# Kernel tuning notes

Measured on AMD Instinct MI355X. Metric: run time of the kernel, lower is better.

Reference implementation:

```python
import jax, jax.numpy as jnp
import numpy as np

B, N, H, W = 4, 4096, 480, 640
RADIUS = 2.0        # hard-coded self.radius in DiskLoss
SCORES_TH = 0.1     # PeakyLoss scores_th
KP_PENALTY = -0.001 # configs['kp_penalty']


def setup_inputs() -> dict:
    key = jax.random.key(0)
    ks = jax.random.split(key, 6)
    lp0 = jax.random.uniform(ks[0], (B, 1, H, W), dtype=jnp.float32)
    lp1 = jax.random.uniform(ks[1], (B, 1, H, W), dtype=jnp.float32)
    # keypoints are normalized grid_sample coords in [-1, 1], (x, y) order
    kp0 = jax.random.uniform(ks[2], (B, N, 2), dtype=jnp.float32) * 2.0 - 1.0
    kp1 = jax.random.uniform(ks[3], (B, N, 2), dtype=jnp.float32) * 2.0 - 1.0
    d0 = jax.random.uniform(ks[4], (B, N), dtype=jnp.float32)
    d1 = jax.random.uniform(ks[5], (B, N), dtype=jnp.float32)
    return dict(local_point0=lp0, local_point1=lp1, keypoints0=kp0,
                keypoints1=kp1, score_dispersity0=d0, score_dispersity1=d1)


def grid_sample_bilinear(img, pts):
    """torch.grid_sample(mode='bilinear', align_corners=True) for one image.
    img: [H, W]; pts: [N, 2] in [-1, 1], pts[:,0]=x (width), pts[:,1]=y (height)."""
    Hh, Ww = img.shape
    x = (pts[:, 0] + 1.0) * 0.5 * (Ww - 1)
    y = (pts[:, 1] + 1.0) * 0.5 * (Hh - 1)
    x0 = jnp.floor(x); y0 = jnp.floor(y)
    wx = x - x0; wy = y - y0
    def g(yy, xx):
        yi = jnp.clip(yy, 0, Hh - 1).astype(jnp.int32)
        xi = jnp.clip(xx, 0, Ww - 1).astype(jnp.int32)
        return img[yi, xi]
    return (g(y0, x0) * (1 - wx) * (1 - wy)
            + g(y0, x0 + 1) * wx * (1 - wy)
            + g(y0 + 1, x0) * (1 - wx) * wy
            + g(y0 + 1, x0 + 1) * wx * wy)


def nms_valid(kpts_wh, scores):
    """Faithful sequential NMS from compute_correspondence for one image.
    kpts_wh: [N, 2] pixel coords; scores: [N]. Returns bool [N] valid mask."""
    n = scores.shape[0]
    sq = jnp.sum(kpts_wh * kpts_wh, axis=-1)
    d2 = sq[:, None] + sq[None, :] - 2.0 * (kpts_wh @ kpts_wh.T)  # [N, N]
    local_mask = d2 < RADIUS * RADIUS
    valid_cnt0 = local_mask.sum(-1).astype(jnp.int32)
    need = valid_cnt0 > 1  # indices_need_nms (computed once, as in torch)
    idx = jnp.arange(n)
    neg_inf = jnp.asarray(-jnp.inf, scores.dtype)
    def body(i, vc):
        row = local_mask[i]
        cond = need[i] & (vc[i] > 0)
        j = jnp.argmax(jnp.where(row, scores, neg_inf))  # best-scoring neighbor
        suppressed = jnp.where(row & (idx != j), 0, vc)
        return jnp.where(cond, suppressed, vc)
    vc = jax.lax.fori_loop(0, n, body, valid_cnt0)
    return vc > 0


def stream_loss(local_point, kpts, disp):
    # local_point [B,1,H,W], kpts [B,N,2] in [-1,1], disp [B,N]
    wh = jnp.array([local_point.shape[3] - 1, local_point.shape[2] - 1],
                   dtype=local_point.dtype)
    scores = jax.vmap(lambda m, k: grid_sample_bilinear(m[0], k))(local_point, kpts)  # [B,N]
    kpts_wh = (kpts / 2.0 + 0.5) * wh  # pixel coords
    valid = jax.vmap(nms_valid)(jax.lax.stop_gradient(kpts_wh),
                                jax.lax.stop_gradient(scores))  # [B,N] bool
    # PeakyLoss over NMS-surviving keypoints with score > threshold
    peaky_mask = (valid & (scores > SCORES_TH)).astype(disp.dtype)
    cnt = jnp.maximum(peaky_mask.sum(), 1.0)
    loss_peaky = jnp.sum(disp * peaky_mask) / cnt
    # keypoint score term (kp_penalty-weighted mean of surviving scores)
    vmask = valid.astype(scores.dtype)
    vcnt = jnp.maximum(vmask.sum(), 1.0)
    score_mean = jnp.sum(scores * vmask) / vcnt
    return loss_peaky + KP_PENALTY * score_mean


def reference(local_point0, local_point1, keypoints0, keypoints1,
              score_dispersity0, score_dispersity1):
    return (stream_loss(local_point0, keypoints0, score_dispersity0)
            + stream_loss(local_point1, keypoints1, score_dispersity1))
```

## Files before the change

kernel.cpp:

```cpp
#include <hip/hip_runtime.h>
#include <math.h>

#define NN 4096
#define HH 480
#define WW 640
#define RAD2 4.0f
#define TH_SCORE 0.1f
#define KPPEN -0.001f
#define CXN 160
#define CYN 120
#define NCELL (CXN * CYN)
#define SLOTS 8
#define CAP 48

#define OFF_SCORES  0
#define OFF_PTS     131072
#define OFF_CNT     655360
#define OFF_PARTNER 688128
#define OFF_ROWS    753664
#define OFF_CELLS   1277952
#define OFF_CCNT    3735552
#define OFF_ACC     4349952
#define OFF_DONE    4349984

__global__ __launch_bounds__(256) void k_sample(
    const float* __restrict__ lp0, const float* __restrict__ lp1,
    const float* __restrict__ kp0, const float* __restrict__ kp1,
    float* __restrict__ scores, float4* __restrict__ pts,
    unsigned short* __restrict__ cells, unsigned int* __restrict__ ccnt)
{
#pragma clang fp contract(off)
    int gid = blockIdx.x * 256 + threadIdx.x;
    int s = gid >> 14;
    int r = gid & 16383;
    int b = r >> 12;
    const float* kp  = (s ? kp1 : kp0) + (size_t)r * 2;
    const float* img = (s ? lp1 : lp0) + (size_t)b * (HH * WW);
    float px = kp[0], py = kp[1];
    float x = (px + 1.0f) * 0.5f * (float)(WW - 1);
    float y = (py + 1.0f) * 0.5f * (float)(HH - 1);
    float x0 = floorf(x), y0 = floorf(y);
    float wx = x - x0, wy = y - y0;
    int ix0 = (int)fminf(fmaxf(x0, 0.0f), (float)(WW - 1));
    int iy0 = (int)fminf(fmaxf(y0, 0.0f), (float)(HH - 1));
    int ix1 = (int)fminf(fmaxf(x0 + 1.0f, 0.0f), (float)(WW - 1));
    int iy1 = (int)fminf(fmaxf(y0 + 1.0f, 0.0f), (float)(HH - 1));
    float g00 = img[iy0 * WW + ix0];
    float g01 = img[iy0 * WW + ix1];
    float g10 = img[iy1 * WW + ix0];
    float g11 = img[iy1 * WW + ix1];
    float sc = g00 * (1.0f - wx) * (1.0f - wy)
             + g01 * wx * (1.0f - wy)
             + g10 * (1.0f - wx) * wy
             + g11 * wx * wy;
    float xw = (px / 2.0f + 0.5f) * (float)(WW - 1);
    float yw = (py / 2.0f + 0.5f) * (float)(HH - 1);
    float sq = xw * xw + yw * yw;
    scores[gid] = sc;
    pts[gid] = make_float4(xw, yw, sq, 0.0f);
    int imgid = gid >> 12;
    int li = gid & (NN - 1);
    int cx = (int)(xw * 0.25f); cx = cx < 0 ? 0 : (cx > CXN - 1 ? CXN - 1 : cx);
    int cy = (int)(yw * 0.25f); cy = cy < 0 ? 0 : (cy > CYN - 1 ? CYN - 1 : cy);
    int cell = imgid * NCELL + cy * CXN + cx;
    unsigned int pos = atomicAdd(&ccnt[cell], 1u);
    if (pos < SLOTS) cells[(size_t)cell * SLOTS + pos] = (unsigned short)li;
}

__global__ __launch_bounds__(256) void k_cnt(
    const float4* __restrict__ pts, const unsigned short* __restrict__ cells,
    const unsigned int* __restrict__ ccnt,
    unsigned char* __restrict__ cnt, unsigned short* __restrict__ partner,
    uint4* __restrict__ rows4)
{
#pragma clang fp contract(off)
    int gid = blockIdx.x * 256 + threadIdx.x;
    int imgid = gid >> 12;
    int li = gid & (NN - 1);
    const float4* p = pts + ((size_t)imgid << 12);
    float4 a = p[li];
    int cx = (int)(a.x * 0.25f); cx = cx < 0 ? 0 : (cx > CXN - 1 ? CXN - 1 : cx);
    int cy = (int)(a.y * 0.25f); cy = cy < 0 ? 0 : (cy > CYN - 1 ? CYN - 1 : cy);

    int c = 0, sum = 0; bool ov = false;
    unsigned long long rlo = 0ull, rhi = 0ull;
    auto place = [&](int pos, unsigned q) {
        unsigned long long v = (unsigned long long)q;
        switch (pos) {
            case 0: rlo |= v;       break;
            case 1: rlo |= v << 16; break;
            case 2: rlo |= v << 32; break;
            case 3: rlo |= v << 48; break;
            case 4: rhi |= v;       break;
            case 5: rhi |= v << 16; break;
            case 6: rhi |= v << 32; break;
            case 7: rhi |= v << 48; break;
        }
    };
    auto test = [&](unsigned q) {
        float4 qq = p[q];
        float dot = a.x * qq.x + a.y * qq.y;
        float t = a.z + qq.z;
        float d2 = fmaf(-2.0f, dot, t);
        if (d2 < RAD2) {
            if (c < 8) place(c, q);
            ++c; sum += (int)q;
        }
    };

#pragma unroll
    for (int dy = -1; dy <= 1; ++dy) {
#pragma unroll
        for (int dx = -1; dx <= 1; ++dx) {
            int yy = cy + dy, xx = cx + dx;
            bool valid = (yy >= 0) & (yy < CYN) & (xx >= 0) & (xx < CXN);
            int cell = imgid * NCELL + (valid ? yy * CXN + xx : 0);
            unsigned n = valid ? ccnt[cell] : 0u;
            if (n > SLOTS) { ov = true; n = SLOTS; }
            uint4 cl = valid ? *(const uint4*)&cells[(size_t)cell * SLOTS]
                             : make_uint4(0, 0, 0, 0);
            unsigned q0 = cl.x & 0xffffu, q1 = cl.x >> 16;
            unsigned q2 = cl.y & 0xffffu, q3 = cl.y >> 16;
            unsigned q4 = cl.z & 0xffffu, q5 = cl.z >> 16;
            unsigned q6 = cl.w & 0xffffu, q7 = cl.w >> 16;
            if (n > 0) test(q0);
            if (n > 1) test(q1);
            if (n > 2) test(q2);
            if (n > 3) test(q3);
            if (n > 4) test(q4);
            if (n > 5) test(q5);
            if (n > 6) test(q6);
            if (n > 7) test(q7);
        }
    }
    if (ov) {
        c = 0; sum = 0; rlo = 0ull; rhi = 0ull;
        for (int j = 0; j < NN; ++j) test((unsigned)j);
    }
    cnt[gid] = (unsigned char)(c > 255 ? 255 : c);
    partner[gid] = (unsigned short)((sum - li) & 0xFFFF);
    if (c >= 3 && c <= 8)
        rows4[gid] = make_uint4((unsigned)rlo, (unsigned)(rlo >> 32),
                                (unsigned)rhi, (unsigned)(rhi >> 32));
}

__global__ __launch_bounds__(256) void k_nms(
    const float* __restrict__ scoresG, const float4* __restrict__ pts,
    const unsigned char* __restrict__ cntG, const unsigned short* __restrict__ partnerG,
    const uint4* __restrict__ rows4,
    const float* __restrict__ dd0, const float* __restrict__ dd1,
    float* __restrict__ acc, unsigned int* __restrict__ done,
    float* __restrict__ out)
{
#pragma clang fp contract(off)
    __shared__ float          s_sc[NN];
    __shared__ unsigned char  s_cnt[NN];
    __shared__ unsigned short s_partner[NN];
    __shared__ unsigned short s_mem[256][CAP + 2];
    __shared__ float s_red[4];

    int imgid = blockIdx.x >> 4;
    int seg = blockIdx.x & 15;
    int base = imgid << 12;
    int tid = threadIdx.x;
    const float4* p = pts + (size_t)base;

    for (int t = tid; t < NN; t += 256) {
        s_sc[t] = scoresG[base + t];
        s_cnt[t] = cntG[base + t];
        s_partner[t] = partnerG[base + t];
    }
    __syncthreads();

    int li = (seg << 8) + tid;
    int c = s_cnt[li];
    bool alive = true;

    if (c >= 2) {
        int pr = s_partner[li];
        if (c == 2 && s_cnt[pr] == 2) {
            int lo = li < pr ? li : pr, hi = li < pr ? pr : li;
            int w = (s_sc[lo] >= s_sc[hi]) ? lo : hi;
            alive = (w == li);
        } else {
            unsigned short* mem = s_mem[tid];
            int cntm = 1, proc = 0;
            mem[0] = (unsigned short)li;
            auto insert = [&](unsigned q) {
                for (int k = 0; k < cntm; ++k) if (mem[k] == (unsigned short)q) return;
                if (cntm < CAP) mem[cntm++] = (unsigned short)q;
            };
            auto full_insert = [&](int m) {
                float4 pm = p[m];
                for (int j = 0; j < NN; ++j) {
                    float4 qq = p[j];
                    float dot = pm.x * qq.x + pm.y * qq.y;
                    float t = pm.z + qq.z;
                    float d2 = fmaf(-2.0f, dot, t);
                    if (d2 < RAD2) insert((unsigned)j);
                }
            };
            while (proc < cntm) {
                int m = mem[proc++];
                int cm = s_cnt[m];
                if (cm == 2) {
                    insert(s_partner[m]);
                } else if (cm <= 8) {
                    uint4 w = rows4[base + m];
                    unsigned q0 = w.x & 0xffffu, q1 = w.x >> 16;
                    unsigned q2 = w.y & 0xffffu, q3 = w.y >> 16;
                    unsigned q4 = w.z & 0xffffu, q5 = w.z >> 16;
                    unsigned q6 = w.w & 0xffffu, q7 = w.w >> 16;
                    if (cm > 0) insert(q0);
                    if (cm > 1) insert(q1);
                    if (cm > 2) insert(q2);
                    if (cm > 3) insert(q3);
                    if (cm > 4) insert(q4);
                    if (cm > 5) insert(q5);
                    if (cm > 6) insert(q6);
                    if (cm > 7) insert(q7);
                } else {
                    full_insert(m);
                }
            }
            for (int k = 1; k < cntm; ++k) {
                unsigned short v = mem[k]; int j2 = k;
                while (j2 > 0 && mem[j2 - 1] > v) { mem[j2] = mem[j2 - 1]; --j2; }
                mem[j2] = v;
            }
            unsigned long long am = (cntm >= 64) ? ~0ull : ((1ull << cntm) - 1ull);
            auto clearbit = [&](unsigned q) {
                for (int k = 0; k < cntm; ++k)
                    if (mem[k] == (unsigned short)q) { am &= ~(1ull << k); return; }
            };
            for (int k = 0; k < cntm; ++k) {
                if (!((am >> k) & 1ull)) continue;
                int m = mem[k];
                int cm = s_cnt[m];
                if (cm == 2) {
                    int pr2 = s_partner[m];
                    int lo = m < pr2 ? m : pr2, hi = m < pr2 ? pr2 : m;
                    int w = (s_sc[lo] >= s_sc[hi]) ? lo : hi;
                    clearbit((unsigned)(w == lo ? hi : lo));
                } else if (cm <= 8) {
                    uint4 w = rows4[base + m];
                    unsigned q0 = w.x & 0xffffu, q1 = w.x >> 16;
                    unsigned q2 = w.y & 0xffffu, q3 = w.y >> 16;
                    unsigned q4 = w.z & 0xffffu, q5 = w.z >> 16;
                    unsigned q6 = w.w & 0xffffu, q7 = w.w >> 16;
                    float bs = -1.0f; int bi = NN;
                    auto cand = [&](int k2, unsigned q) {
                        if (k2 < cm) {
                            float s2 = s_sc[q];
                            if (s2 > bs || (s2 == bs && (int)q < bi)) { bs = s2; bi = (int)q; }
                        }
                    };
                    cand(0, q0); cand(1, q1); cand(2, q2); cand(3, q3);
                    cand(4, q4); cand(5, q5); cand(6, q6); cand(7, q7);
                    auto clr = [&](int k2, unsigned q) {
                        if (k2 < cm && (int)q != bi) clearbit(q);
                    };
                    clr(0, q0); clr(1, q1); clr(2, q2); clr(3, q3);
                    clr(4, q4); clr(5, q5); clr(6, q6); clr(7, q7);
                } else {
                    float4 pm = p[m];
                    float bs = -1.0f; int bi = NN;
                    for (int j = 0; j < NN; ++j) {
                        float4 qq = p[j];
                        float dot = pm.x * qq.x + pm.y * qq.y;
                        float t = pm.z + qq.z;
                        float d2 = fmaf(-2.0f, dot, t);
                        if (d2 < RAD2) {
                            float s2 = s_sc[j];
                            if (s2 > bs || (s2 == bs && j < bi)) { bs = s2; bi = j; }
                        }
                    }
                    for (int j = 0; j < NN; ++j) {
                        float4 qq = p[j];
                        float dot = pm.x * qq.x + pm.y * qq.y;
                        float t = pm.z + qq.z;
                        float d2 = fmaf(-2.0f, dot, t);
                        if (d2 < RAD2 && j != bi) clearbit((unsigned)j);
                    }
                }
            }
            for (int k = 0; k < cntm; ++k)
                if (mem[k] == (unsigned short)li) { alive = ((am >> k) & 1ull) != 0; break; }
        }
    }

    int stream = imgid >> 2, b = imgid & 3;
    const float* disp = (stream ? dd1 : dd0) + (size_t)b * NN;
    float sum_dp = 0.f, cnt_p = 0.f, sum_sv = 0.f, cnt_v = 0.f;
    if (alive) {
        float sc = s_sc[li];
        cnt_v = 1.0f; sum_sv = sc;
        if (sc > TH_SCORE) { cnt_p = 1.0f; sum_dp = disp[li]; }
    }
    __syncthreads();
#pragma unroll
    for (int q = 0; q < 4; ++q) {
        float v = (q == 0) ? sum_dp : (q == 1) ? cnt_p : (q == 2) ? sum_sv : cnt_v;
        for (int o = 32; o > 0; o >>= 1) v += __shfl_down(v, o, 64);
        if ((tid & 63) == 0) s_red[tid >> 6] = v;
        __syncthreads();
        if (tid == 0) {
            float r = s_red[0] + s_red[1] + s_red[2] + s_red[3];
            atomicAdd(&acc[stream * 4 + q], r);
        }
        __syncthreads();
    }

    if (tid == 0) {
        __threadfence();
        unsigned prev = atomicAdd(done, 1u);
        if (prev == 127u) {
            float r = 0.0f;
            for (int s = 0; s < 2; ++s) {
                float sdp = atomicAdd(&acc[s * 4 + 0], 0.0f);
                float cp  = atomicAdd(&acc[s * 4 + 1], 0.0f);
                float ssv = atomicAdd(&acc[s * 4 + 2], 0.0f);
                float cv  = atomicAdd(&acc[s * 4 + 3], 0.0f);
                r += sdp / fmaxf(cp, 1.0f) + KPPEN * (ssv / fmaxf(cv, 1.0f));
            }
            out[0] = r;
        }
    }
}

extern "C" void kernel_launch(void* const* d_in, const int* in_sizes, int n_in,
                              void* d_out, int out_size, void* d_ws, size_t ws_size,
                              hipStream_t stream)
{
    const float* lp0 = (const float*)d_in[0];
    const float* lp1 = (const float*)d_in[1];
    const float* kp0 = (const float*)d_in[2];
    const float* kp1 = (const float*)d_in[3];
    const float* dd0 = (const float*)d_in[4];
    const float* dd1 = (const float*)d_in[5];

    char* ws = (char*)d_ws;
    float*          scores  = (float*)(ws + OFF_SCORES);
    float4*         pts     = (float4*)(ws + OFF_PTS);
    unsigned char*  cnt     = (unsigned char*)(ws + OFF_CNT);
    unsigned short* partner = (unsigned short*)(ws + OFF_PARTNER);
    uint4*          rows4   = (uint4*)(ws + OFF_ROWS);
    unsigned short* cells   = (unsigned short*)(ws + OFF_CELLS);
    unsigned int*   ccnt    = (unsigned int*)(ws + OFF_CCNT);
    float*          acc     = (float*)(ws + OFF_ACC);
    unsigned int*   done    = (unsigned int*)(ws + OFF_DONE);

    hipMemsetAsync(ws + OFF_CCNT, 0, 614436, stream);
    k_sample<<<128, 256, 0, stream>>>(lp0, lp1, kp0, kp1, scores, pts, cells, ccnt);
    k_cnt<<<128, 256, 0, stream>>>(pts, cells, ccnt, cnt, partner, rows4);
    k_nms<<<128, 256, 0, stream>>>(scores, pts, cnt, partner, rows4,
                                   dd0, dd1, acc, done, (float*)d_out);
}
```

Baseline: 116.3 us.

## Fuse three NMS pipeline kernels into one cooperative kernel with grid syncs

Merges the sampling, neighbour-counting and NMS kernels into a single cooperative launch, using grid-wide syncs in place of kernel boundaries. The final reduction now runs after a last grid sync instead of through a done-counter atomic. The aim is to remove the launch gaps between three short kernels. In exchange it pays the cost of cooperative launch and grid barriers, and the large shared-memory footprint now applies to every phase.

```diff
diff --git a/kernel.cpp b/kernel.cpp
--- a/kernel.cpp
+++ b/kernel.cpp
@@ -1,5 +1,8 @@
 #include <hip/hip_runtime.h>
+#include <hip/hip_cooperative_groups.h>
 #include <math.h>
+
+namespace cg = cooperative_groups;
 
 #define NN 4096
 #define HH 480
@@ -12,6 +15,7 @@
 #define NCELL (CXN * CYN)
 #define SLOTS 8
 #define CAP 48
+#define NBLK 128
 
 #define OFF_SCORES  0
 #define OFF_PTS     131072
@@ -21,135 +25,15 @@
 #define OFF_CELLS   1277952
 #define OFF_CCNT    3735552
 #define OFF_ACC     4349952
-#define OFF_DONE    4349984
-
-__global__ __launch_bounds__(256) void k_sample(
+
+__global__ __launch_bounds__(256) void k_fused(
     const float* __restrict__ lp0, const float* __restrict__ lp1,
     const float* __restrict__ kp0, const float* __restrict__ kp1,
+    const float* __restrict__ dd0, const float* __restrict__ dd1,
     float* __restrict__ scores, float4* __restrict__ pts,
-    unsigned short* __restrict__ cells, unsigned int* __restrict__ ccnt)
-{
-#pragma clang fp contract(off)
-    int gid = blockIdx.x * 256 + threadIdx.x;
-    int s = gid >> 14;
-    int r = gid & 16383;
-    int b = r >> 12;
-    const float* kp  = (s ? kp1 : kp0) + (size_t)r * 2;
-    const float* img = (s ? lp1 : lp0) + (size_t)b * (HH * WW);
-    float px = kp[0], py = kp[1];
-    float x = (px + 1.0f) * 0.5f * (float)(WW - 1);
-    float y = (py + 1.0f) * 0.5f * (float)(HH - 1);
-    float x0 = floorf(x), y0 = floorf(y);
-    float wx = x - x0, wy = y - y0;
-    int ix0 = (int)fminf(fmaxf(x0, 0.0f), (float)(WW - 1));
-    int iy0 = (int)fminf(fmaxf(y0, 0.0f), (float)(HH - 1));
-    int ix1 = (int)fminf(fmaxf(x0 + 1.0f, 0.0f), (float)(WW - 1));
-    int iy1 = (int)fminf(fmaxf(y0 + 1.0f, 0.0f), (float)(HH - 1));
-    float g00 = img[iy0 * WW + ix0];
-    float g01 = img[iy0 * WW + ix1];
-    float g10 = img[iy1 * WW + ix0];
-    float g11 = img[iy1 * WW + ix1];
-    float sc = g00 * (1.0f - wx) * (1.0f - wy)
-             + g01 * wx * (1.0f - wy)
-             + g10 * (1.0f - wx) * wy
-             + g11 * wx * wy;
-    float xw = (px / 2.0f + 0.5f) * (float)(WW - 1);
-    float yw = (py / 2.0f + 0.5f) * (float)(HH - 1);
-    float sq = xw * xw + yw * yw;
-    scores[gid] = sc;
-    pts[gid] = make_float4(xw, yw, sq, 0.0f);
-    int imgid = gid >> 12;
-    int li = gid & (NN - 1);
-    int cx = (int)(xw * 0.25f); cx = cx < 0 ? 0 : (cx > CXN - 1 ? CXN - 1 : cx);
-    int cy = (int)(yw * 0.25f); cy = cy < 0 ? 0 : (cy > CYN - 1 ? CYN - 1 : cy);
-    int cell = imgid * NCELL + cy * CXN + cx;
-    unsigned int pos = atomicAdd(&ccnt[cell], 1u);
-    if (pos < SLOTS) cells[(size_t)cell * SLOTS + pos] = (unsigned short)li;
-}
-
-__global__ __launch_bounds__(256) void k_cnt(
-    const float4* __restrict__ pts, const unsigned short* __restrict__ cells,
-    const unsigned int* __restrict__ ccnt,
     unsigned char* __restrict__ cnt, unsigned short* __restrict__ partner,
-    uint4* __restrict__ rows4)
-{
-#pragma clang fp contract(off)
-    int gid = blockIdx.x * 256 + threadIdx.x;
-    int imgid = gid >> 12;
-    int li = gid & (NN - 1);
-    const float4* p = pts + ((size_t)imgid << 12);
-    float4 a = p[li];
-    int cx = (int)(a.x * 0.25f); cx = cx < 0 ? 0 : (cx > CXN - 1 ? CXN - 1 : cx);
-    int cy = (int)(a.y * 0.25f); cy = cy < 0 ? 0 : (cy > CYN - 1 ? CYN - 1 : cy);
-
-    int c = 0, sum = 0; bool ov = false;
-    unsigned long long rlo = 0ull, rhi = 0ull;
-    auto place = [&](int pos, unsigned q) {
-        unsigned long long v = (unsigned long long)q;
-        switch (pos) {
-            case 0: rlo |= v;       break;
-            case 1: rlo |= v << 16; break;
-            case 2: rlo |= v << 32; break;
-            case 3: rlo |= v << 48; break;
-            case 4: rhi |= v;       break;
-            case 5: rhi |= v << 16; break;
-            case 6: rhi |= v << 32; break;
-            case 7: rhi |= v << 48; break;
-        }
-    };
-    auto test = [&](unsigned q) {
-        float4 qq = p[q];
-        float dot = a.x * qq.x + a.y * qq.y;
-        float t = a.z + qq.z;
-        float d2 = fmaf(-2.0f, dot, t);
-        if (d2 < RAD2) {
-            if (c < 8) place(c, q);
-            ++c; sum += (int)q;
-        }
-    };
-
-#pragma unroll
-    for (int dy = -1; dy <= 1; ++dy) {
-#pragma unroll
-        for (int dx = -1; dx <= 1; ++dx) {
-            int yy = cy + dy, xx = cx + dx;
-            bool valid = (yy >= 0) & (yy < CYN) & (xx >= 0) & (xx < CXN);
-            int cell = imgid * NCELL + (valid ? yy * CXN + xx : 0);
-            unsigned n = valid ? ccnt[cell] : 0u;
-            if (n > SLOTS) { ov = true; n = SLOTS; }
-            uint4 cl = valid ? *(const uint4*)&cells[(size_t)cell * SLOTS]
-                             : make_uint4(0, 0, 0, 0);
-            unsigned q0 = cl.x & 0xffffu, q1 = cl.x >> 16;
-            unsigned q2 = cl.y & 0xffffu, q3 = cl.y >> 16;
-            unsigned q4 = cl.z & 0xffffu, q5 = cl.z >> 16;
-            unsigned q6 = cl.w & 0xffffu, q7 = cl.w >> 16;
-            if (n > 0) test(q0);
-            if (n > 1) test(q1);
-            if (n > 2) test(q2);
-            if (n > 3) test(q3);
-            if (n > 4) test(q4);
-            if (n > 5) test(q5);
-            if (n > 6) test(q6);
-            if (n > 7) test(q7);
-        }
-    }
-    if (ov) {
-        c = 0; sum = 0; rlo = 0ull; rhi = 0ull;
-        for (int j = 0; j < NN; ++j) test((unsigned)j);
-    }
-    cnt[gid] = (unsigned char)(c > 255 ? 255 : c);
-    partner[gid] = (unsigned short)((sum - li) & 0xFFFF);
-    if (c >= 3 && c <= 8)
-        rows4[gid] = make_uint4((unsigned)rlo, (unsigned)(rlo >> 32),
-                                (unsigned)rhi, (unsigned)(rhi >> 32));
-}
-
-__global__ __launch_bounds__(256) void k_nms(
-    const float* __restrict__ scoresG, const float4* __restrict__ pts,
-    const unsigned char* __restrict__ cntG, const unsigned short* __restrict__ partnerG,
-    const uint4* __restrict__ rows4,
-    const float* __restrict__ dd0, const float* __restrict__ dd1,
-    float* __restrict__ acc, unsigned int* __restrict__ done,
+    uint4* __restrict__ rows4, unsigned short* __restrict__ cells,
+    unsigned int* __restrict__ ccnt, float* __restrict__ acc,
     float* __restrict__ out)
 {
 #pragma clang fp contract(off)
@@ -159,172 +43,279 @@
     __shared__ unsigned short s_mem[256][CAP + 2];
     __shared__ float s_red[4];
 
-    int imgid = blockIdx.x >> 4;
-    int seg = blockIdx.x & 15;
-    int base = imgid << 12;
+    cg::grid_group grid = cg::this_grid();
     int tid = threadIdx.x;
-    const float4* p = pts + (size_t)base;
-
-    for (int t = tid; t < NN; t += 256) {
-        s_sc[t] = scoresG[base + t];
-        s_cnt[t] = cntG[base + t];
-        s_partner[t] = partnerG[base + t];
+    int gid = blockIdx.x * 256 + tid;
+
+    {
+        int s = gid >> 14;
+        int r = gid & 16383;
+        int b = r >> 12;
+        const float* kp  = (s ? kp1 : kp0) + (size_t)r * 2;
+        const float* img = (s ? lp1 : lp0) + (size_t)b * (HH * WW);
+        float px = kp[0], py = kp[1];
+        float x = (px + 1.0f) * 0.5f * (float)(WW - 1);
+        float y = (py + 1.0f) * 0.5f * (float)(HH - 1);
+        float x0 = floorf(x), y0 = floorf(y);
+        float wx = x - x0, wy = y - y0;
+        int ix0 = (int)fminf(fmaxf(x0, 0.0f), (float)(WW - 1));
+        int iy0 = (int)fminf(fmaxf(y0, 0.0f), (float)(HH - 1));
+        int ix1 = (int)fminf(fmaxf(x0 + 1.0f, 0.0f), (float)(WW - 1));
+        int iy1 = (int)fminf(fmaxf(y0 + 1.0f, 0.0f), (float)(HH - 1));
+        float g00 = img[iy0 * WW + ix0];
+        float g01 = img[iy0 * WW + ix1];
+        float g10 = img[iy1 * WW + ix0];
+        float g11 = img[iy1 * WW + ix1];
+        float sc = g00 * (1.0f - wx) * (1.0f - wy)
+                 + g01 * wx * (1.0f - wy)
+                 + g10 * (1.0f - wx) * wy
+                 + g11 * wx * wy;
+        float xw = (px / 2.0f + 0.5f) * (float)(WW - 1);
+        float yw = (py / 2.0f + 0.5f) * (float)(HH - 1);
+        float sq = xw * xw + yw * yw;
+        scores[gid] = sc;
+        pts[gid] = make_float4(xw, yw, sq, 0.0f);
+        int imgid = gid >> 12;
+        int li = gid & (NN - 1);
+        int cx = (int)(xw * 0.25f); cx = cx < 0 ? 0 : (cx > CXN - 1 ? CXN - 1 : cx);
+        int cy = (int)(yw * 0.25f); cy = cy < 0 ? 0 : (cy > CYN - 1 ? CYN - 1 : cy);
+        int cell = imgid * NCELL + cy * CXN + cx;
+        unsigned int pos = atomicAdd(&ccnt[cell], 1u);
+        if (pos < SLOTS) cells[(size_t)cell * SLOTS + pos] = (unsigned short)li;
     }
-    __syncthreads();
-
-    int li = (seg << 8) + tid;
-    int c = s_cnt[li];
-    bool alive = true;
-
-    if (c >= 2) {
-        int pr = s_partner[li];
-        if (c == 2 && s_cnt[pr] == 2) {
-            int lo = li < pr ? li : pr, hi = li < pr ? pr : li;
-            int w = (s_sc[lo] >= s_sc[hi]) ? lo : hi;
-            alive = (w == li);
-        } else {
-            unsigned short* mem = s_mem[tid];
-            int cntm = 1, proc = 0;
-            mem[0] = (unsigned short)li;
-            auto insert = [&](unsigned q) {
-                for (int k = 0; k < cntm; ++k) if (mem[k] == (unsigned short)q) return;
-                if (cntm < CAP) mem[cntm++] = (unsigned short)q;
-            };
-            auto full_insert = [&](int m) {
-                float4 pm = p[m];
-                for (int j = 0; j < NN; ++j) {
-                    float4 qq = p[j];
-                    float dot = pm.x * qq.x + pm.y * qq.y;
-                    float t = pm.z + qq.z;
-                    float d2 = fmaf(-2.0f, dot, t);
-                    if (d2 < RAD2) insert((unsigned)j);
-                }
-            };
-            while (proc < cntm) {
-                int m = mem[proc++];
-                int cm = s_cnt[m];
-                if (cm == 2) {
-                    insert(s_partner[m]);
-                } else if (cm <= 8) {
-                    uint4 w = rows4[base + m];
-                    unsigned q0 = w.x & 0xffffu, q1 = w.x >> 16;
-                    unsigned q2 = w.y & 0xffffu, q3 = w.y >> 16;
-                    unsigned q4 = w.z & 0xffffu, q5 = w.z >> 16;
-                    unsigned q6 = w.w & 0xffffu, q7 = w.w >> 16;
-                    if (cm > 0) insert(q0);
-                    if (cm > 1) insert(q1);
-                    if (cm > 2) insert(q2);
-                    if (cm > 3) insert(q3);
-                    if (cm > 4) insert(q4);
-                    if (cm > 5) insert(q5);
-                    if (cm > 6) insert(q6);
-                    if (cm > 7) insert(q7);
-                } else {
-                    full_insert(m);
-                }
-            }
-            for (int k = 1; k < cntm; ++k) {
-                unsigned short v = mem[k]; int j2 = k;
-                while (j2 > 0 && mem[j2 - 1] > v) { mem[j2] = mem[j2 - 1]; --j2; }
-                mem[j2] = v;
-            }
-            unsigned long long am = (cntm >= 64) ? ~0ull : ((1ull << cntm) - 1ull);
-            auto clearbit = [&](unsigned q) {
-                for (int k = 0; k < cntm; ++k)
-                    if (mem[k] == (unsigned short)q) { am &= ~(1ull << k); return; }
-            };
-            for (int k = 0; k < cntm; ++k) {
-                if (!((am >> k) & 1ull)) continue;
-                int m = mem[k];
-                int cm = s_cnt[m];
-                if (cm == 2) {
-                    int pr2 = s_partner[m];
-                    int lo = m < pr2 ? m : pr2, hi = m < pr2 ? pr2 : m;
-                    int w = (s_sc[lo] >= s_sc[hi]) ? lo : hi;
-                    clearbit((unsigned)(w == lo ? hi : lo));
-                } else if (cm <= 8) {
-                    uint4 w = rows4[base + m];
-                    unsigned q0 = w.x & 0xffffu, q1 = w.x >> 16;
-                    unsigned q2 = w.y & 0xffffu, q3 = w.y >> 16;
-                    unsigned q4 = w.z & 0xffffu, q5 = w.z >> 16;
-                    unsigned q6 = w.w & 0xffffu, q7 = w.w >> 16;
-                    float bs = -1.0f; int bi = NN;
-                    auto cand = [&](int k2, unsigned q) {
-                        if (k2 < cm) {
-                            float s2 = s_sc[q];
-                            if (s2 > bs || (s2 == bs && (int)q < bi)) { bs = s2; bi = (int)q; }
-                        }
-                    };
-                    cand(0, q0); cand(1, q1); cand(2, q2); cand(3, q3);
-                    cand(4, q4); cand(5, q5); cand(6, q6); cand(7, q7);
-                    auto clr = [&](int k2, unsigned q) {
-                        if (k2 < cm && (int)q != bi) clearbit(q);
-                    };
-                    clr(0, q0); clr(1, q1); clr(2, q2); clr(3, q3);
-                    clr(4, q4); clr(5, q5); clr(6, q6); clr(7, q7);
-                } else {
+    grid.sync();
+
+    {
+        int imgid = gid >> 12;
+        int li = gid & (NN - 1);
+        const float4* p = pts + ((size_t)imgid << 12);
+        float4 a = p[li];
+        int cx = (int)(a.x * 0.25f); cx = cx < 0 ? 0 : (cx > CXN - 1 ? CXN - 1 : cx);
+        int cy = (int)(a.y * 0.25f); cy = cy < 0 ? 0 : (cy > CYN - 1 ? CYN - 1 : cy);
+
+        int c = 0, sum = 0; bool ov = false;
+        unsigned long long rlo = 0ull, rhi = 0ull;
+        auto place = [&](int pos, unsigned q) {
+            unsigned long long v = (unsigned long long)q;
+            switch (pos) {
+                case 0: rlo |= v;       break;
+                case 1: rlo |= v << 16; break;
+                case 2: rlo |= v << 32; break;
+                case 3: rlo |= v << 48; break;
+                case 4: rhi |= v;       break;
+                case 5: rhi |= v << 16; break;
+                case 6: rhi |= v << 32; break;
+                case 7: rhi |= v << 48; break;
+            }
+        };
+        auto test = [&](unsigned q) {
+            float4 qq = p[q];
+            float dot = a.x * qq.x + a.y * qq.y;
+            float t = a.z + qq.z;
+            float d2 = fmaf(-2.0f, dot, t);
+            if (d2 < RAD2) {
+                if (c < 8) place(c, q);
+                ++c; sum += (int)q;
+            }
+        };
+#pragma unroll
+        for (int dy = -1; dy <= 1; ++dy) {
+#pragma unroll
+            for (int dx = -1; dx <= 1; ++dx) {
+                int yy = cy + dy, xx = cx + dx;
+                bool valid = (yy >= 0) & (yy < CYN) & (xx >= 0) & (xx < CXN);
+                int cell = imgid * NCELL + (valid ? yy * CXN + xx : 0);
+                unsigned n = valid ? ccnt[cell] : 0u;
+                if (n > SLOTS) { ov = true; n = SLOTS; }
+                uint4 cl = valid ? *(const uint4*)&cells[(size_t)cell * SLOTS]
+                                 : make_uint4(0, 0, 0, 0);
+                unsigned q0 = cl.x & 0xffffu, q1 = cl.x >> 16;
+                unsigned q2 = cl.y & 0xffffu, q3 = cl.y >> 16;
+                unsigned q4 = cl.z & 0xffffu, q5 = cl.z >> 16;
+                unsigned q6 = cl.w & 0xffffu, q7 = cl.w >> 16;
+                if (n > 0) test(q0);
+                if (n > 1) test(q1);
+                if (n > 2) test(q2);
+                if (n > 3) test(q3);
+                if (n > 4) test(q4);
+                if (n > 5) test(q5);
+                if (n > 6) test(q6);
+                if (n > 7) test(q7);
+            }
+        }
+        if (ov) {
+            c = 0; sum = 0; rlo = 0ull; rhi = 0ull;
+            for (int j = 0; j < NN; ++j) test((unsigned)j);
+        }
+        cnt[gid] = (unsigned char)(c > 255 ? 255 : c);
+        partner[gid] = (unsigned short)((sum - li) & 0xFFFF);
+        if (c >= 3 && c <= 8)
+            rows4[gid] = make_uint4((unsigned)rlo, (unsigned)(rlo >> 32),
+                                    (unsigned)rhi, (unsigned)(rhi >> 32));
+    }
+    grid.sync();
+
+    {
+        int imgid = gid >> 12;
+        int li = gid & (NN - 1);
+        int base = imgid << 12;
+        const float4* p = pts + (size_t)base;
+
+        for (int t = tid; t < NN; t += 256) {
+            s_sc[t] = scores[base + t];
+            s_cnt[t] = cnt[base + t];
+            s_partner[t] = partner[base + t];
+        }
+        __syncthreads();
+
+        int c = s_cnt[li];
+        bool alive = true;
+
+        if (c >= 2) {
+            int pr = s_partner[li];
+            if (c == 2 && s_cnt[pr] == 2) {
+                int lo = li < pr ? li : pr, hi = li < pr ? pr : li;
+                int w = (s_sc[lo] >= s_sc[hi]) ? lo : hi;
+                alive = (w == li);
+            } else {
+                unsigned short* mem = s_mem[tid];
+                int cntm = 1, proc = 0;
+                mem[0] = (unsigned short)li;
+                auto insert = [&](unsigned q) {
+                    for (int k = 0; k < cntm; ++k) if (mem[k] == (unsigned short)q) return;
+                    if (cntm < CAP) mem[cntm++] = (unsigned short)q;
+                };
+                auto full_insert = [&](int m) {
                     float4 pm = p[m];
-                    float bs = -1.0f; int bi = NN;
                     for (int j = 0; j < NN; ++j) {
                         float4 qq = p[j];
                         float dot = pm.x * qq.x + pm.y * qq.y;
                         float t = pm.z + qq.z;
                         float d2 = fmaf(-2.0f, dot, t);
-                        if (d2 < RAD2) {
-                            float s2 = s_sc[j];
-                            if (s2 > bs || (s2 == bs && j < bi)) { bs = s2; bi = j; }
+                        if (d2 < RAD2) insert((unsigned)j);
+                    }
+                };
+                while (proc < cntm) {
+                    int m = mem[proc++];
+                    int cm = s_cnt[m];
+                    if (cm == 2) {
+                        insert(s_partner[m]);
+                    } else if (cm <= 8) {
+                        uint4 w = rows4[base + m];
+                        unsigned q0 = w.x & 0xffffu, q1 = w.x >> 16;
+                        unsigned q2 = w.y & 0xffffu, q3 = w.y >> 16;
+                        unsigned q4 = w.z & 0xffffu, q5 = w.z >> 16;
+                        unsigned q6 = w.w & 0xffffu, q7 = w.w >> 16;
+                        if (cm > 0) insert(q0);
+                        if (cm > 1) insert(q1);
+                        if (cm > 2) insert(q2);
+                        if (cm > 3) insert(q3);
+                        if (cm > 4) insert(q4);
+                        if (cm > 5) insert(q5);
+                        if (cm > 6) insert(q6);
+                        if (cm > 7) insert(q7);
+                    } else {
+                        full_insert(m);
+                    }
+                }
+                for (int k = 1; k < cntm; ++k) {
+                    unsigned short v = mem[k]; int j2 = k;
+                    while (j2 > 0 && mem[j2 - 1] > v) { mem[j2] = mem[j2 - 1]; --j2; }
+                    mem[j2] = v;
+                }
+                unsigned long long am = (cntm >= 64) ? ~0ull : ((1ull << cntm) - 1ull);
+                auto clearbit = [&](unsigned q) {
+                    for (int k = 0; k < cntm; ++k)
+                        if (mem[k] == (unsigned short)q) { am &= ~(1ull << k); return; }
+                };
+                for (int k = 0; k < cntm; ++k) {
+                    if (!((am >> k) & 1ull)) continue;
+                    int m = mem[k];
+                    int cm = s_cnt[m];
+                    if (cm == 2) {
+                        int pr2 = s_partner[m];
+                        int lo = m < pr2 ? m : pr2, hi = m < pr2 ? pr2 : m;
+                        int w = (s_sc[lo] >= s_sc[hi]) ? lo : hi;
+                        clearbit((unsigned)(w == lo ? hi : lo));
+                    } else if (cm <= 8) {
+                        uint4 w = rows4[base + m];
+                        unsigned q0 = w.x & 0xffffu, q1 = w.x >> 16;
+                        unsigned q2 = w.y & 0xffffu, q3 = w.y >> 16;
+                        unsigned q4 = w.z & 0xffffu, q5 = w.z >> 16;
+                        unsigned q6 = w.w & 0xffffu, q7 = w.w >> 16;
+                        float bs = -1.0f; int bi = NN;
+                        auto cand = [&](int k2, unsigned q) {
+                            if (k2 < cm) {
+                                float s2 = s_sc[q];
+                                if (s2 > bs || (s2 == bs && (int)q < bi)) { bs = s2; bi = (int)q; }
+                            }
+                        };
+                        cand(0, q0); cand(1, q1); cand(2, q2); cand(3, q3);
+                        cand(4, q4); cand(5, q5); cand(6, q6); cand(7, q7);
+                        auto clr = [&](int k2, unsigned q) {
+                            if (k2 < cm && (int)q != bi) clearbit(q);
+                        };
+                        clr(0, q0); clr(1, q1); clr(2, q2); clr(3, q3);
+                        clr(4, q4); clr(5, q5); clr(6, q6); clr(7, q7);
+                    } else {
+                        float4 pm = p[m];
+                        float bs = -1.0f; int bi = NN;
+                        for (int j = 0; j < NN; ++j) {
+                            float4 qq = p[j];
+                            float dot = pm.x * qq.x + pm.y * qq.y;
+                            float t = pm.z + qq.z;
+                            float d2 = fmaf(-2.0f, dot, t);
+                            if (d2 < RAD2) {
+                                float s2 = s_sc[j];
+                                if (s2 > bs || (s2 == bs && j < bi)) { bs = s2; bi = j; }
+                            }
+                        }
+                        for (int j = 0; j < NN; ++j) {
+                            float4 qq = p[j];
+                            float dot = pm.x * qq.x + pm.y * qq.y;
+                            float t = pm.z + qq.z;
+                            float d2 = fmaf(-2.0f, dot, t);
+                            if (d2 < RAD2 && j != bi) clearbit((unsigned)j);
                         }
                     }
-                    for (int j = 0; j < NN; ++j) {
-                        float4 qq = p[j];
-                        float dot = pm.x * qq.x + pm.y * qq.y;
-                        float t = pm.z + qq.z;
-                        float d2 = fmaf(-2.0f, dot, t);
-                        if (d2 < RAD2 && j != bi) clearbit((unsigned)j);
-                    }
                 }
-            }
-            for (int k = 0; k < cntm; ++k)
-                if (mem[k] == (unsigned short)li) { alive = ((am >> k) & 1ull) != 0; break; }
+                for (int k = 0; k < cntm; ++k)
+                    if (mem[k] == (unsigned short)li) { alive = ((am >> k) & 1ull) != 0; break; }
+            }
+        }
+
+        int stream = imgid >> 2, b = imgid & 3;
+        const float* disp = (stream ? dd1 : dd0) + (size_t)b * NN;
+        float sum_dp = 0.f, cnt_p = 0.f, sum_sv = 0.f, cnt_v = 0.f;
+        if (alive) {
+            float sc = s_sc[li];
+            cnt_v = 1.0f; sum_sv = sc;
+            if (sc > TH_SCORE) { cnt_p = 1.0f; sum_dp = disp[li]; }
+        }
+        __syncthreads();
+#pragma unroll
+        for (int q = 0; q < 4; ++q) {
+            float v = (q == 0) ? sum_dp : (q == 1) ? cnt_p : (q == 2) ? sum_sv : cnt_v;
+            for (int o = 32; o > 0; o >>= 1) v += __shfl_down(v, o, 64);
+            if ((tid & 63) == 0) s_red[tid >> 6] = v;
+            __syncthreads();
+            if (tid == 0) {
+                float r = s_red[0] + s_red[1] + s_red[2] + s_red[3];
+                atomicAdd(&acc[stream * 4 + q], r);
+            }
+            __syncthreads();
         }
     }
-
-    int stream = imgid >> 2, b = imgid & 3;
-    const float* disp = (stream ? dd1 : dd0) + (size_t)b * NN;
-    float sum_dp = 0.f, cnt_p = 0.f, sum_sv = 0.f, cnt_v = 0.f;
-    if (alive) {
-        float sc = s_sc[li];
-        cnt_v = 1.0f; sum_sv = sc;
-        if (sc > TH_SCORE) { cnt_p = 1.0f; sum_dp = disp[li]; }
-    }
-    __syncthreads();
-#pragma unroll
-    for (int q = 0; q < 4; ++q) {
-        float v = (q == 0) ? sum_dp : (q == 1) ? cnt_p : (q == 2) ? sum_sv : cnt_v;
-        for (int o = 32; o > 0; o >>= 1) v += __shfl_down(v, o, 64);
-        if ((tid & 63) == 0) s_red[tid >> 6] = v;
-        __syncthreads();
-        if (tid == 0) {
-            float r = s_red[0] + s_red[1] + s_red[2] + s_red[3];
-            atomicAdd(&acc[stream * 4 + q], r);
-        }
-        __syncthreads();
-    }
-
-    if (tid == 0) {
-        __threadfence();
-        unsigned prev = atomicAdd(done, 1u);
-        if (prev == 127u) {
-            float r = 0.0f;
-            for (int s = 0; s < 2; ++s) {
-                float sdp = atomicAdd(&acc[s * 4 + 0], 0.0f);
-                float cp  = atomicAdd(&acc[s * 4 + 1], 0.0f);
-                float ssv = atomicAdd(&acc[s * 4 + 2], 0.0f);
-                float cv  = atomicAdd(&acc[s * 4 + 3], 0.0f);
-                r += sdp / fmaxf(cp, 1.0f) + KPPEN * (ssv / fmaxf(cv, 1.0f));
-            }
-            out[0] = r;
-        }
+    grid.sync();
+
+    if (blockIdx.x == 0 && tid == 0) {
+        float r = 0.0f;
+        for (int s = 0; s < 2; ++s) {
+            float sdp = acc[s * 4 + 0], cp = acc[s * 4 + 1];
+            float ssv = acc[s * 4 + 2], cv = acc[s * 4 + 3];
+            r += sdp / fmaxf(cp, 1.0f) + KPPEN * (ssv / fmaxf(cv, 1.0f));
+        }
+        out[0] = r;
     }
 }
 
@@ -348,11 +339,13 @@
     unsigned short* cells   = (unsigned short*)(ws + OFF_CELLS);
     unsigned int*   ccnt    = (unsigned int*)(ws + OFF_CCNT);
     float*          acc     = (float*)(ws + OFF_ACC);
-    unsigned int*   done    = (unsigned int*)(ws + OFF_DONE);
-
-    hipMemsetAsync(ws + OFF_CCNT, 0, 614436, stream);
-    k_sample<<<128, 256, 0, stream>>>(lp0, lp1, kp0, kp1, scores, pts, cells, ccnt);
-    k_cnt<<<128, 256, 0, stream>>>(pts, cells, ccnt, cnt, partner, rows4);
-    k_nms<<<128, 256, 0, stream>>>(scores, pts, cnt, partner, rows4,
-                                   dd0, dd1, acc, done, (float*)d_out);
+    float*          outp    = (float*)d_out;
+
+    hipMemsetAsync(ws + OFF_CCNT, 0, 614432, stream);
+
+    void* args[] = { &lp0, &lp1, &kp0, &kp1, &dd0, &dd1,
+                     &scores, &pts, &cnt, &partner, &rows4,
+                     &cells, &ccnt, &acc, &outp };
+    hipLaunchCooperativeKernel((void*)k_fused, dim3(NBLK), dim3(256),
+                               args, 0, stream);
 }
```

Measured after the change: 169.4 us. 1.46x slower.

## Split NMS into fast trivial pass and compacted residual worklist kernel

Applied to the files above, without the earlier changes.

The NMS kernel now resolves isolated and mutual-pair keypoints directly from global arrays and appends everything else to an atomic worklist. A new small-block kernel processes only the worklist entries with the component-walk NMS, reading scores and counts from global memory instead of shared memory, and performs the final reduction. The aim is to remove the divergence and shared-memory staging that cost every thread in the old kernel, and to spread the rare expensive cases across many small blocks. The price is an extra launch, worklist atomics, and uncached global reads in the residual path.

```diff
diff --git a/kernel.cpp b/kernel.cpp
--- a/kernel.cpp
+++ b/kernel.cpp
@@ -12,6 +12,7 @@
 #define NCELL (CXN * CYN)
 #define SLOTS 8
 #define CAP 48
+#define RESBLK 64
 
 #define OFF_SCORES  0
 #define OFF_PTS     131072
@@ -22,6 +23,8 @@
 #define OFF_CCNT    3735552
 #define OFF_ACC     4349952
 #define OFF_DONE    4349984
+#define OFF_WLN     4349988
+#define OFF_WL      4349992
 
 __global__ __launch_bounds__(256) void k_sample(
     const float* __restrict__ lp0, const float* __restrict__ lp1,
@@ -107,7 +110,6 @@
             ++c; sum += (int)q;
         }
     };
-
 #pragma unroll
     for (int dy = -1; dy <= 1; ++dy) {
 #pragma unroll
@@ -145,155 +147,45 @@
 }
 
 __global__ __launch_bounds__(256) void k_nms(
-    const float* __restrict__ scoresG, const float4* __restrict__ pts,
-    const unsigned char* __restrict__ cntG, const unsigned short* __restrict__ partnerG,
-    const uint4* __restrict__ rows4,
+    const float* __restrict__ scoresG, const unsigned char* __restrict__ cntG,
+    const unsigned short* __restrict__ partnerG,
     const float* __restrict__ dd0, const float* __restrict__ dd1,
-    float* __restrict__ acc, unsigned int* __restrict__ done,
-    float* __restrict__ out)
+    unsigned int* __restrict__ wl_n, int* __restrict__ wl,
+    float* __restrict__ acc)
 {
-#pragma clang fp contract(off)
-    __shared__ float          s_sc[NN];
-    __shared__ unsigned char  s_cnt[NN];
-    __shared__ unsigned short s_partner[NN];
-    __shared__ unsigned short s_mem[256][CAP + 2];
     __shared__ float s_red[4];
-
-    int imgid = blockIdx.x >> 4;
-    int seg = blockIdx.x & 15;
+    int tid = threadIdx.x;
+    int gid = blockIdx.x * 256 + tid;
+    int imgid = gid >> 12;
+    int li = gid & (NN - 1);
     int base = imgid << 12;
-    int tid = threadIdx.x;
-    const float4* p = pts + (size_t)base;
-
-    for (int t = tid; t < NN; t += 256) {
-        s_sc[t] = scoresG[base + t];
-        s_cnt[t] = cntG[base + t];
-        s_partner[t] = partnerG[base + t];
-    }
-    __syncthreads();
-
-    int li = (seg << 8) + tid;
-    int c = s_cnt[li];
-    bool alive = true;
-
-    if (c >= 2) {
-        int pr = s_partner[li];
-        if (c == 2 && s_cnt[pr] == 2) {
+
+    int c = cntG[gid];
+    bool alive = true, residual = false;
+    if (c >= 3) {
+        residual = true;
+    } else if (c == 2) {
+        int pr = partnerG[gid];
+        if (cntG[base + pr] == 2) {
+            float sl = scoresG[gid], sp = scoresG[base + pr];
             int lo = li < pr ? li : pr, hi = li < pr ? pr : li;
-            int w = (s_sc[lo] >= s_sc[hi]) ? lo : hi;
+            float slo = li < pr ? sl : sp, shi = li < pr ? sp : sl;
+            int w = (slo >= shi) ? lo : hi;
             alive = (w == li);
         } else {
-            unsigned short* mem = s_mem[tid];
-            int cntm = 1, proc = 0;
-            mem[0] = (unsigned short)li;
-            auto insert = [&](unsigned q) {
-                for (int k = 0; k < cntm; ++k) if (mem[k] == (unsigned short)q) return;
-                if (cntm < CAP) mem[cntm++] = (unsigned short)q;
-            };
-            auto full_insert = [&](int m) {
-                float4 pm = p[m];
-                for (int j = 0; j < NN; ++j) {
-                    float4 qq = p[j];
-                    float dot = pm.x * qq.x + pm.y * qq.y;
-                    float t = pm.z + qq.z;
-                    float d2 = fmaf(-2.0f, dot, t);
-                    if (d2 < RAD2) insert((unsigned)j);
-                }
-            };
-            while (proc < cntm) {
-                int m = mem[proc++];
-                int cm = s_cnt[m];
-                if (cm == 2) {
-                    insert(s_partner[m]);
-                } else if (cm <= 8) {
-                    uint4 w = rows4[base + m];
-                    unsigned q0 = w.x & 0xffffu, q1 = w.x >> 16;
-                    unsigned q2 = w.y & 0xffffu, q3 = w.y >> 16;
-                    unsigned q4 = w.z & 0xffffu, q5 = w.z >> 16;
-                    unsigned q6 = w.w & 0xffffu, q7 = w.w >> 16;
-                    if (cm > 0) insert(q0);
-                    if (cm > 1) insert(q1);
-                    if (cm > 2) insert(q2);
-                    if (cm > 3) insert(q3);
-                    if (cm > 4) insert(q4);
-                    if (cm > 5) insert(q5);
-                    if (cm > 6) insert(q6);
-                    if (cm > 7) insert(q7);
-                } else {
-                    full_insert(m);
-                }
-            }
-            for (int k = 1; k < cntm; ++k) {
-                unsigned short v = mem[k]; int j2 = k;
-                while (j2 > 0 && mem[j2 - 1] > v) { mem[j2] = mem[j2 - 1]; --j2; }
-                mem[j2] = v;
-            }
-            unsigned long long am = (cntm >= 64) ? ~0ull : ((1ull << cntm) - 1ull);
-            auto clearbit = [&](unsigned q) {
-                for (int k = 0; k < cntm; ++k)
-                    if (mem[k] == (unsigned short)q) { am &= ~(1ull << k); return; }
-            };
-            for (int k = 0; k < cntm; ++k) {
-                if (!((am >> k) & 1ull)) continue;
-                int m = mem[k];
-                int cm = s_cnt[m];
-                if (cm == 2) {
-                    int pr2 = s_partner[m];
-                    int lo = m < pr2 ? m : pr2, hi = m < pr2 ? pr2 : m;
-                    int w = (s_sc[lo] >= s_sc[hi]) ? lo : hi;
-                    clearbit((unsigned)(w == lo ? hi : lo));
-                } else if (cm <= 8) {
-                    uint4 w = rows4[base + m];
-                    unsigned q0 = w.x & 0xffffu, q1 = w.x >> 16;
-                    unsigned q2 = w.y & 0xffffu, q3 = w.y >> 16;
-                    unsigned q4 = w.z & 0xffffu, q5 = w.z >> 16;
-                    unsigned q6 = w.w & 0xffffu, q7 = w.w >> 16;
-                    float bs = -1.0f; int bi = NN;
-                    auto cand = [&](int k2, unsigned q) {
-                        if (k2 < cm) {
-                            float s2 = s_sc[q];
-                            if (s2 > bs || (s2 == bs && (int)q < bi)) { bs = s2; bi = (int)q; }
-                        }
-                    };
-                    cand(0, q0); cand(1, q1); cand(2, q2); cand(3, q3);
-                    cand(4, q4); cand(5, q5); cand(6, q6); cand(7, q7);
-                    auto clr = [&](int k2, unsigned q) {
-                        if (k2 < cm && (int)q != bi) clearbit(q);
-                    };
-                    clr(0, q0); clr(1, q1); clr(2, q2); clr(3, q3);
-                    clr(4, q4); clr(5, q5); clr(6, q6); clr(7, q7);
-                } else {
-                    float4 pm = p[m];
-                    float bs = -1.0f; int bi = NN;
-                    for (int j = 0; j < NN; ++j) {
-                        float4 qq = p[j];
-                        float dot = pm.x * qq.x + pm.y * qq.y;
-                        float t = pm.z + qq.z;
-                        float d2 = fmaf(-2.0f, dot, t);
-                        if (d2 < RAD2) {
-                            float s2 = s_sc[j];
-                            if (s2 > bs || (s2 == bs && j < bi)) { bs = s2; bi = j; }
-                        }
-                    }
-                    for (int j = 0; j < NN; ++j) {
-                        float4 qq = p[j];
-                        float dot = pm.x * qq.x + pm.y * qq.y;
-                        float t = pm.z + qq.z;
-                        float d2 = fmaf(-2.0f, dot, t);
-                        if (d2 < RAD2 && j != bi) clearbit((unsigned)j);
-                    }
-                }
-            }
-            for (int k = 0; k < cntm; ++k)
-                if (mem[k] == (unsigned short)li) { alive = ((am >> k) & 1ull) != 0; break; }
-        }
+            residual = true;
+        }
+    }
+    if (residual) {
+        unsigned pos = atomicAdd(wl_n, 1u);
+        wl[pos] = gid;
     }
 
     int stream = imgid >> 2, b = imgid & 3;
     const float* disp = (stream ? dd1 : dd0) + (size_t)b * NN;
     float sum_dp = 0.f, cnt_p = 0.f, sum_sv = 0.f, cnt_v = 0.f;
-    if (alive) {
-        float sc = s_sc[li];
+    if (!residual && alive) {
+        float sc = scoresG[gid];
         cnt_v = 1.0f; sum_sv = sc;
         if (sc > TH_SCORE) { cnt_p = 1.0f; sum_dp = disp[li]; }
     }
@@ -310,11 +202,165 @@
         }
         __syncthreads();
     }
+}
+
+__global__ __launch_bounds__(RESBLK) void k_res(
+    const float* __restrict__ scoresG, const float4* __restrict__ pts,
+    const unsigned char* __restrict__ cntG, const unsigned short* __restrict__ partnerG,
+    const uint4* __restrict__ rows4,
+    const float* __restrict__ dd0, const float* __restrict__ dd1,
+    const unsigned int* __restrict__ wl_n, const int* __restrict__ wl,
+    float* __restrict__ acc, unsigned int* __restrict__ done,
+    float* __restrict__ out)
+{
+#pragma clang fp contract(off)
+    __shared__ unsigned short s_mem[RESBLK][CAP + 2];
+    int tid = threadIdx.x;
+    int n = (int)*wl_n;
+    float a_dp = 0.f, a_cp = 0.f, a_sv = 0.f, a_cv = 0.f;
+    float b_dp = 0.f, b_cp = 0.f, b_sv = 0.f, b_cv = 0.f;
+
+    for (int t = blockIdx.x * RESBLK + tid; t < n; t += gridDim.x * RESBLK) {
+        int gid = wl[t];
+        int imgid = gid >> 12;
+        int li = gid & (NN - 1);
+        int base = imgid << 12;
+        const float4* p = pts + (size_t)base;
+
+        unsigned short* mem = s_mem[tid];
+        int cntm = 1, proc = 0;
+        mem[0] = (unsigned short)li;
+        auto insert = [&](unsigned q) {
+            for (int k = 0; k < cntm; ++k) if (mem[k] == (unsigned short)q) return;
+            if (cntm < CAP) mem[cntm++] = (unsigned short)q;
+        };
+        auto full_insert = [&](int m) {
+            float4 pm = p[m];
+            for (int j = 0; j < NN; ++j) {
+                float4 qq = p[j];
+                float dot = pm.x * qq.x + pm.y * qq.y;
+                float tt = pm.z + qq.z;
+                float d2 = fmaf(-2.0f, dot, tt);
+                if (d2 < RAD2) insert((unsigned)j);
+            }
+        };
+        while (proc < cntm) {
+            int m = mem[proc++];
+            int cm = cntG[base + m];
+            if (cm == 2) {
+                insert(partnerG[base + m]);
+            } else if (cm <= 8) {
+                uint4 w = rows4[base + m];
+                unsigned q0 = w.x & 0xffffu, q1 = w.x >> 16;
+                unsigned q2 = w.y & 0xffffu, q3 = w.y >> 16;
+                unsigned q4 = w.z & 0xffffu, q5 = w.z >> 16;
+                unsigned q6 = w.w & 0xffffu, q7 = w.w >> 16;
+                if (cm > 0) insert(q0);
+                if (cm > 1) insert(q1);
+                if (cm > 2) insert(q2);
+                if (cm > 3) insert(q3);
+                if (cm > 4) insert(q4);
+                if (cm > 5) insert(q5);
+                if (cm > 6) insert(q6);
+                if (cm > 7) insert(q7);
+            } else {
+                full_insert(m);
+            }
+        }
+        for (int k = 1; k < cntm; ++k) {
+            unsigned short v = mem[k]; int j2 = k;
+            while (j2 > 0 && mem[j2 - 1] > v) { mem[j2] = mem[j2 - 1]; --j2; }
+            mem[j2] = v;
+        }
+        unsigned long long am = (cntm >= 64) ? ~0ull : ((1ull << cntm) - 1ull);
+        auto clearbit = [&](unsigned q) {
+            for (int k = 0; k < cntm; ++k)
+                if (mem[k] == (unsigned short)q) { am &= ~(1ull << k); return; }
+        };
+        for (int k = 0; k < cntm; ++k) {
+            if (!((am >> k) & 1ull)) continue;
+            int m = mem[k];
+            int cm = cntG[base + m];
+            if (cm == 2) {
+                int pr2 = partnerG[base + m];
+                int lo = m < pr2 ? m : pr2, hi = m < pr2 ? pr2 : m;
+                float slo = scoresG[base + lo], shi = scoresG[base + hi];
+                int w = (slo >= shi) ? lo : hi;
+                clearbit((unsigned)(w == lo ? hi : lo));
+            } else if (cm <= 8) {
+                uint4 w = rows4[base + m];
+                unsigned q0 = w.x & 0xffffu, q1 = w.x >> 16;
+                unsigned q2 = w.y & 0xffffu, q3 = w.y >> 16;
+                unsigned q4 = w.z & 0xffffu, q5 = w.z >> 16;
+                unsigned q6 = w.w & 0xffffu, q7 = w.w >> 16;
+                float bs = -1.0f; int bi = NN;
+                auto cand = [&](int k2, unsigned q) {
+                    if (k2 < cm) {
+                        float s2 = scoresG[base + q];
+                        if (s2 > bs || (s2 == bs && (int)q < bi)) { bs = s2; bi = (int)q; }
+                    }
+                };
+                cand(0, q0); cand(1, q1); cand(2, q2); cand(3, q3);
+                cand(4, q4); cand(5, q5); cand(6, q6); cand(7, q7);
+                auto clr = [&](int k2, unsigned q) {
+                    if (k2 < cm && (int)q != bi) clearbit(q);
+                };
+                clr(0, q0); clr(1, q1); clr(2, q2); clr(3, q3);
+                clr(4, q4); clr(5, q5); clr(6, q6); clr(7, q7);
+            } else {
+                float4 pm = p[m];
+                float bs = -1.0f; int bi = NN;
+                for (int j = 0; j < NN; ++j) {
+                    float4 qq = p[j];
+                    float dot = pm.x * qq.x + pm.y * qq.y;
+                    float tt = pm.z + qq.z;
+                    float d2 = fmaf(-2.0f, dot, tt);
+                    if (d2 < RAD2) {
+                        float s2 = scoresG[base + j];
+                        if (s2 > bs || (s2 == bs && j < bi)) { bs = s2; bi = j; }
+                    }
+                }
+                for (int j = 0; j < NN; ++j) {
+                    float4 qq = p[j];
+                    float dot = pm.x * qq.x + pm.y * qq.y;
+                    float tt = pm.z + qq.z;
+                    float d2 = fmaf(-2.0f, dot, tt);
+                    if (d2 < RAD2 && j != bi) clearbit((unsigned)j);
+                }
+            }
+        }
+        bool alive = false;
+        for (int k = 0; k < cntm; ++k)
+            if (mem[k] == (unsigned short)li) { alive = ((am >> k) & 1ull) != 0; break; }
+
+        if (alive) {
+            float sc = scoresG[gid];
+            int stream = imgid >> 2, b = imgid & 3;
+            const float* disp = (stream ? dd1 : dd0) + (size_t)b * NN;
+            float dp = 0.f, cp = 0.f;
+            if (sc > TH_SCORE) { dp = disp[li]; cp = 1.0f; }
+            if (stream == 0) { a_sv += sc; a_cv += 1.0f; a_dp += dp; a_cp += cp; }
+            else             { b_sv += sc; b_cv += 1.0f; b_dp += dp; b_cp += cp; }
+        }
+    }
+
+    auto wred = [&](float v) {
+        for (int o = 32; o > 0; o >>= 1) v += __shfl_down(v, o, 64);
+        return v;
+    };
+    a_dp = wred(a_dp); a_cp = wred(a_cp); a_sv = wred(a_sv); a_cv = wred(a_cv);
+    b_dp = wred(b_dp); b_cp = wred(b_cp); b_sv = wred(b_sv); b_cv = wred(b_cv);
+    if (tid == 0) {
+        atomicAdd(&acc[0], a_dp); atomicAdd(&acc[1], a_cp);
+        atomicAdd(&acc[2], a_sv); atomicAdd(&acc[3], a_cv);
+        atomicAdd(&acc[4], b_dp); atomicAdd(&acc[5], b_cp);
+        atomicAdd(&acc[6], b_sv); atomicAdd(&acc[7], b_cv);
+    }
 
     if (tid == 0) {
         __threadfence();
         unsigned prev = atomicAdd(done, 1u);
-        if (prev == 127u) {
+        if (prev == gridDim.x - 1) {
             float r = 0.0f;
             for (int s = 0; s < 2; ++s) {
                 float sdp = atomicAdd(&acc[s * 4 + 0], 0.0f);
@@ -349,10 +395,14 @@
     unsigned int*   ccnt    = (unsigned int*)(ws + OFF_CCNT);
     float*          acc     = (float*)(ws + OFF_ACC);
     unsigned int*   done    = (unsigned int*)(ws + OFF_DONE);
-
-    hipMemsetAsync(ws + OFF_CCNT, 0, 614436, stream);
+    unsigned int*   wl_n    = (unsigned int*)(ws + OFF_WLN);
+    int*            wl      = (int*)(ws + OFF_WL);
+
+    hipMemsetAsync(ws + OFF_CCNT, 0, 614440, stream);
     k_sample<<<128, 256, 0, stream>>>(lp0, lp1, kp0, kp1, scores, pts, cells, ccnt);
     k_cnt<<<128, 256, 0, stream>>>(pts, cells, ccnt, cnt, partner, rows4);
-    k_nms<<<128, 256, 0, stream>>>(scores, pts, cnt, partner, rows4,
-                                   dd0, dd1, acc, done, (float*)d_out);
+    k_nms<<<128, 256, 0, stream>>>(scores, cnt, partner, dd0, dd1, wl_n, wl, acc);
+    k_res<<<64, RESBLK, 0, stream>>>(scores, pts, cnt, partner, rows4,
+                                     dd0, dd1, wl_n, wl, acc, done,
+                                     (float*)d_out);
 }
```

New measurement: 141.5 us. 1.22x slower.
